# Kernel optimization log

Measured on AMD Instinct MI355X. Metric: run time of the kernel, lower is better.

Reference implementation:

```python
import jax, jax.numpy as jnp
import numpy as np

EPS = 1e-08


def squash(s):
    # s: [B, out_caps, out_d]
    s2 = jnp.sum(s * s, axis=-1, keepdims=True)
    return s2 / (1.0 + s2) * (s / jnp.sqrt(s2 + EPS))


def setup_inputs() -> dict:
    key = jax.random.key(0)
    k1, k2 = jax.random.split(key)
    B, in_caps, out_caps, in_d, out_d = 128, 1152, 32, 8, 16
    u = jax.random.normal(k1, (B, in_caps, in_d), dtype=jnp.float32)
    weight = jax.random.normal(k2, (in_caps, out_caps, in_d, out_d), dtype=jnp.float32)
    return {"u": u, "weight": weight, "iterations": 3}


def reference(u, weight, iterations):
    # u: [B, in_caps, in_d]; weight: [in_caps, out_caps, in_d, out_d]
    u_hat = jnp.einsum('ijnm,bin->bijm', weight, u)  # [B, i, j, m]
    B, in_caps, out_caps, _ = u_hat.shape
    b = jnp.zeros((B, in_caps, out_caps), dtype=u.dtype)
    v = None
    for _ in range(iterations):
        c = jax.nn.softmax(b, axis=1)  # faithful to torch code: softmax over in_caps
        s = jnp.einsum('bij,bijm->bjm', c, u_hat)
        v = squash(s)
        a = jnp.einsum('bjm,bijm->bij', v, u_hat)
        b = b + a
    return v
```

## Files before the change

### kernel.cpp

```cpp
#include <hip/hip_runtime.h>
#include <stdint.h>

constexpr int B_SZ     = 128;
constexpr int IN_CAPS  = 1152;
constexpr int OUT_CAPS = 32;
constexpr int IN_D     = 8;
constexpr int OUT_D    = 16;
constexpr int ITERS    = 3;

constexpr int THREADS  = 1024;
constexpr int NW       = THREADS / 64;
constexpr int G        = 2;
constexpr int TILE_R   = 128;
constexpr int NTILE    = IN_CAPS / TILE_R;
constexpr int ROW_F    = 128;

typedef const uint32_t __attribute__((address_space(1)))* gptr_t;
typedef uint32_t       __attribute__((address_space(3)))* lptr_t;
__device__ __forceinline__ void async_copy16(const float* g, float* l) {
    __builtin_amdgcn_global_load_lds((gptr_t)g, (lptr_t)l, 16, 0, 0);
}

__global__ __launch_bounds__(THREADS) void caps_route(
    const float* __restrict__ u,
    const float* __restrict__ w,
    float* __restrict__ out)
{
    __shared__ __align__(16) float tile[TILE_R * ROW_F];
    __shared__ float red_es[NW * 8];
    __shared__ __align__(16) float red_m[NW * 8 * 4];

    const int nwg = gridDim.x;
    const int bid = blockIdx.x;
    const int wid = (bid & 7) * (nwg >> 3) + (bid >> 3);
    const int j   = wid >> 6;
    const int b0  = (wid & 63) * G;

    const int tid  = threadIdx.x;
    const int lane = tid & 63;
    const int wv   = tid >> 6;
    const int bl   = tid & 1;
    const int mq   = (tid >> 1) & 3;
    const int ir   = tid >> 3;
    const int b    = b0 + bl;

    const int pmir = (ir & 7) ^ ((ir & 1) << 2);
    const int o0   = ((mq ^ pmir) << 2);
    const int o1   = (((4 | mq) ^ pmir) << 2);

    float uh[NTILE][4];
    float4 uA0, uA1;

    #define STAGE_TILE(T)                                                     \
    do {                                                                      \
        _Pragma("unroll")                                                     \
        for (int q = 0; q < 4; ++q) {                                         \
            const int Lb   = (wv * 4 + q) * 64;      \
            const int L    = Lb + lane;                                       \
            const int row  = L >> 5;                                          \
            const int slot = L & 31;                                          \
            const int c    = slot ^ ((row & 7) ^ ((row & 1) << 2));           \
            const float* gsrc = w +                                           \
                ((size_t)(((T) * TILE_R + row) * OUT_CAPS + j) * ROW_F + c * 4); \
            async_copy16(gsrc, &tile[Lb * 4]);                                \
        }                                                                     \
    } while (0)

    #define ULOAD(T)                                                          \
    do {                                                                      \
        const float* up = u + ((size_t)b * IN_CAPS + (T) * TILE_R + ir) * IN_D; \
        uA0 = *reinterpret_cast<const float4*>(up);                           \
        uA1 = *reinterpret_cast<const float4*>(up + 4);                       \
    } while (0)

    #define COMP_TILE(T)                                                      \
    do {                                                                      \
        const float* trow = &tile[ir * ROW_F];                                \
        const float uc[8] = {uA0.x, uA0.y, uA0.z, uA0.w,                      \
                             uA1.x, uA1.y, uA1.z, uA1.w};                     \
        float4 acc = make_float4(0.f, 0.f, 0.f, 0.f);                         \
        _Pragma("unroll")                                                     \
        for (int t = 0; t < 4; ++t) {                                         \
            const float4 wa = *reinterpret_cast<const float4*>(trow + t * 32 + o0); \
            const float4 wb = *reinterpret_cast<const float4*>(trow + t * 32 + o1); \
            acc.x = fmaf(uc[2*t], wa.x, acc.x);                               \
            acc.y = fmaf(uc[2*t], wa.y, acc.y);                               \
            acc.z = fmaf(uc[2*t], wa.z, acc.z);                               \
            acc.w = fmaf(uc[2*t], wa.w, acc.w);                               \
            acc.x = fmaf(uc[2*t+1], wb.x, acc.x);                             \
            acc.y = fmaf(uc[2*t+1], wb.y, acc.y);                             \
            acc.z = fmaf(uc[2*t+1], wb.z, acc.z);                             \
            acc.w = fmaf(uc[2*t+1], wb.w, acc.w);                             \
        }                                                                     \
        uh[(T)][0] = acc.x; uh[(T)][1] = acc.y;                               \
        uh[(T)][2] = acc.z; uh[(T)][3] = acc.w;                               \
    } while (0)

    #define STEP(T)                                                           \
    do {                                                                      \
        __syncthreads();                                                      \
        STAGE_TILE(T);                                                        \
        ULOAD(T);                                                             \
        __syncthreads();                                                      \
        COMP_TILE(T);                                                         \
    } while (0)

    STAGE_TILE(0);
    ULOAD(0);
    __syncthreads();
    COMP_TILE(0);
    STEP(1); STEP(2); STEP(3); STEP(4);
    STEP(5); STEP(6); STEP(7); STEP(8);
    #undef STEP
    #undef COMP_TILE
    #undef ULOAD
    #undef STAGE_TILE

    float e[NTILE];
    #pragma unroll
    for (int r = 0; r < NTILE; ++r) e[r] = 1.0f;
    float vv[4];
    const int grp = lane & 7;

    for (int it = 0; it < ITERS; ++it) {
        float esum = 0.0f;
        #pragma unroll
        for (int r = 0; r < NTILE; ++r) esum += e[r];
        esum += __shfl_xor(esum, 8);
        esum += __shfl_xor(esum, 16);
        esum += __shfl_xor(esum, 32);

        float sp0 = 0.f, sp1 = 0.f, sp2 = 0.f, sp3 = 0.f;
        #pragma unroll
        for (int r = 0; r < NTILE; ++r) {
            sp0 = fmaf(e[r], uh[r][0], sp0);
            sp1 = fmaf(e[r], uh[r][1], sp1);
            sp2 = fmaf(e[r], uh[r][2], sp2);
            sp3 = fmaf(e[r], uh[r][3], sp3);
        }
        sp0 += __shfl_xor(sp0, 8);  sp1 += __shfl_xor(sp1, 8);
        sp2 += __shfl_xor(sp2, 8);  sp3 += __shfl_xor(sp3, 8);
        sp0 += __shfl_xor(sp0, 16); sp1 += __shfl_xor(sp1, 16);
        sp2 += __shfl_xor(sp2, 16); sp3 += __shfl_xor(sp3, 16);
        sp0 += __shfl_xor(sp0, 32); sp1 += __shfl_xor(sp1, 32);
        sp2 += __shfl_xor(sp2, 32); sp3 += __shfl_xor(sp3, 32);

        if (lane < 8) {
            red_es[wv * 8 + lane] = esum;
            *reinterpret_cast<float4*>(&red_m[(wv * 8 + lane) * 4]) =
                make_float4(sp0, sp1, sp2, sp3);
        }
        __syncthreads();
        float gsum = 0.0f;
        float sa0 = 0.f, sa1 = 0.f, sa2 = 0.f, sa3 = 0.f;
        #pragma unroll
        for (int q = 0; q < NW; ++q) {
            gsum += red_es[q * 8 + grp];
            const float4 rm =
                *reinterpret_cast<const float4*>(&red_m[(q * 8 + grp) * 4]);
            sa0 += rm.x; sa1 += rm.y; sa2 += rm.z; sa3 += rm.w;
        }
        __syncthreads();

        const float cinv = 1.0f / gsum;
        vv[0] = sa0 * cinv; vv[1] = sa1 * cinv;
        vv[2] = sa2 * cinv; vv[3] = sa3 * cinv;
        float s2 = fmaf(vv[0], vv[0], fmaf(vv[1], vv[1],
                   fmaf(vv[2], vv[2], vv[3] * vv[3])));
        s2 += __shfl_xor(s2, 2);
        s2 += __shfl_xor(s2, 4);
        const float scale = (s2 / (1.0f + s2)) * rsqrtf(s2 + 1e-8f);
        vv[0] *= scale; vv[1] *= scale; vv[2] *= scale; vv[3] *= scale;

        if (it < ITERS - 1) {
            #pragma unroll
            for (int r = 0; r < NTILE; ++r) {
                float a = fmaf(vv[0], uh[r][0], fmaf(vv[1], uh[r][1],
                          fmaf(vv[2], uh[r][2], vv[3] * uh[r][3])));
                a += __shfl_xor(a, 2);
                a += __shfl_xor(a, 4);
                e[r] *= __expf(a);
            }
        }
    }

    if (tid < 8) {
        float4* op = reinterpret_cast<float4*>(
            out + ((size_t)(b0 + bl) * OUT_CAPS + j) * OUT_D + mq * 4);
        *op = make_float4(vv[0], vv[1], vv[2], vv[3]);
    }
}

extern "C" void kernel_launch(void* const* d_in, const int* in_sizes, int n_in,
                              void* d_out, int out_size, void* d_ws, size_t ws_size,
                              hipStream_t stream) {
    const float* u = (const float*)d_in[0];
    const float* w = (const float*)d_in[1];
    float* out     = (float*)d_out;
    (void)in_sizes; (void)n_in; (void)out_size; (void)d_ws; (void)ws_size;

    dim3 grid(OUT_CAPS * (B_SZ / G));
    dim3 block(THREADS);
    hipLaunchKernelGGL(caps_route, grid, block, 0, stream, u, w, out);
}
```

Measured before the change: 175.0 us.

## Double-buffer weight tiles in LDS as packed bf16 with register staging

```diff
diff --git a/kernel.cpp b/kernel.cpp
--- a/kernel.cpp
+++ b/kernel.cpp
@@ -4,7 +4,6 @@
 constexpr int B_SZ     = 128;
 constexpr int IN_CAPS  = 1152;
 constexpr int OUT_CAPS = 32;
-constexpr int IN_D     = 8;
 constexpr int OUT_D    = 16;
 constexpr int ITERS    = 3;
 
@@ -13,22 +12,15 @@
 constexpr int G        = 2;
 constexpr int TILE_R   = 128;
 constexpr int NTILE    = IN_CAPS / TILE_R;
-constexpr int ROW_F    = 128;
-
-typedef const uint32_t __attribute__((address_space(1)))* gptr_t;
-typedef uint32_t       __attribute__((address_space(3)))* lptr_t;
-__device__ __forceinline__ void async_copy16(const float* g, float* l) {
-    __builtin_amdgcn_global_load_lds((gptr_t)g, (lptr_t)l, 16, 0, 0);
-}
 
 __global__ __launch_bounds__(THREADS) void caps_route(
     const float* __restrict__ u,
     const float* __restrict__ w,
     float* __restrict__ out)
 {
-    __shared__ __align__(16) float tile[TILE_R * ROW_F];
-    __shared__ float red_es[NW * 8];
-    __shared__ __align__(16) float red_m[NW * 8 * 4];
+    __shared__ __align__(16) uint32_t tile[2][TILE_R * 64];
+    __shared__ float red_es[8 * NW];
+    __shared__ __align__(16) float red_m[8 * NW * 4];
 
     const int nwg = gridDim.x;
     const int bid = blockIdx.x;
@@ -42,79 +34,92 @@
     const int bl   = tid & 1;
     const int mq   = (tid >> 1) & 3;
     const int ir   = tid >> 3;
+    const int ir3  = ir & 7;
     const int b    = b0 + bl;
 
-    const int pmir = (ir & 7) ^ ((ir & 1) << 2);
-    const int o0   = ((mq ^ pmir) << 2);
-    const int o1   = (((4 | mq) ^ pmir) << 2);
+    const int srow = tid >> 3;
+    const int sc0  = tid & 7;
 
     float uh[NTILE][4];
-    float4 uA0, uA1;
-
-    #define STAGE_TILE(T)                                                     \
-    do {                                                                      \
-        _Pragma("unroll")                                                     \
-        for (int q = 0; q < 4; ++q) {                                         \
-            const int Lb   = (wv * 4 + q) * 64;      \
-            const int L    = Lb + lane;                                       \
-            const int row  = L >> 5;                                          \
-            const int slot = L & 31;                                          \
-            const int c    = slot ^ ((row & 7) ^ ((row & 1) << 2));           \
-            const float* gsrc = w +                                           \
-                ((size_t)(((T) * TILE_R + row) * OUT_CAPS + j) * ROW_F + c * 4); \
-            async_copy16(gsrc, &tile[Lb * 4]);                                \
-        }                                                                     \
-    } while (0)
-
-    #define ULOAD(T)                                                          \
-    do {                                                                      \
-        const float* up = u + ((size_t)b * IN_CAPS + (T) * TILE_R + ir) * IN_D; \
-        uA0 = *reinterpret_cast<const float4*>(up);                           \
-        uA1 = *reinterpret_cast<const float4*>(up + 4);                       \
-    } while (0)
-
-    #define COMP_TILE(T)                                                      \
-    do {                                                                      \
-        const float* trow = &tile[ir * ROW_F];                                \
-        const float uc[8] = {uA0.x, uA0.y, uA0.z, uA0.w,                      \
-                             uA1.x, uA1.y, uA1.z, uA1.w};                     \
-        float4 acc = make_float4(0.f, 0.f, 0.f, 0.f);                         \
+
+    #define GLOADS(T, C2, RA, RB)                                             \
+    do {                                                                      \
+        const float* gb = w +                                                 \
+            (((size_t)((T) * TILE_R + srow) * OUT_CAPS + j) << 7);            \
+        const int t_ = (C2) >> 2, mqs = (C2) & 3;                             \
+        RA = *reinterpret_cast<const float4*>(gb + t_ * 32 + mqs * 4);        \
+        RB = *reinterpret_cast<const float4*>(gb + t_ * 32 + mqs * 4 + 16);   \
+    } while (0)
+
+    #define PACK_WRITE(NB, C2, RA, RB)                                        \
+    do {                                                                      \
+        uint32_t d0, d1, d2, d3;                                              \
+        asm("v_cvt_pk_bf16_f32 %0, %1, %2" : "=v"(d0) : "v"(RA.x), "v"(RB.x));\
+        asm("v_cvt_pk_bf16_f32 %0, %1, %2" : "=v"(d1) : "v"(RA.y), "v"(RB.y));\
+        asm("v_cvt_pk_bf16_f32 %0, %1, %2" : "=v"(d2) : "v"(RA.z), "v"(RB.z));\
+        asm("v_cvt_pk_bf16_f32 %0, %1, %2" : "=v"(d3) : "v"(RA.w), "v"(RB.w));\
+        const int c_ = (C2) ^ (srow & 7);                                     \
+        *reinterpret_cast<uint4*>(&tile[(NB)][(srow * 16 + c_) * 4]) =        \
+            make_uint4(d0, d1, d2, d3);                                       \
+    } while (0)
+
+    #define COMP(NB, T)                                                       \
+    do {                                                                      \
+        const float* up = u + ((size_t)b * IN_CAPS + (T) * TILE_R + ir) * 8;  \
+        const float4 u0 = *reinterpret_cast<const float4*>(up);               \
+        const float4 u1 = *reinterpret_cast<const float4*>(up + 4);           \
+        const float uc[8] = {u0.x, u0.y, u0.z, u0.w, u1.x, u1.y, u1.z, u1.w}; \
+        float a0 = 0.f, a1 = 0.f, a2 = 0.f, a3 = 0.f;                         \
         _Pragma("unroll")                                                     \
         for (int t = 0; t < 4; ++t) {                                         \
-            const float4 wa = *reinterpret_cast<const float4*>(trow + t * 32 + o0); \
-            const float4 wb = *reinterpret_cast<const float4*>(trow + t * 32 + o1); \
-            acc.x = fmaf(uc[2*t], wa.x, acc.x);                               \
-            acc.y = fmaf(uc[2*t], wa.y, acc.y);                               \
-            acc.z = fmaf(uc[2*t], wa.z, acc.z);                               \
-            acc.w = fmaf(uc[2*t], wa.w, acc.w);                               \
-            acc.x = fmaf(uc[2*t+1], wb.x, acc.x);                             \
-            acc.y = fmaf(uc[2*t+1], wb.y, acc.y);                             \
-            acc.z = fmaf(uc[2*t+1], wb.z, acc.z);                             \
-            acc.w = fmaf(uc[2*t+1], wb.w, acc.w);                             \
+            const int c_ = ((t << 2) | mq) ^ ir3;                             \
+            const uint4 d = *reinterpret_cast<const uint4*>(                  \
+                &tile[(NB)][(ir * 16 + c_) * 4]);                             \
+            const float ue = uc[2 * t], uo = uc[2 * t + 1];                   \
+            a0 = fmaf(ue, __uint_as_float(d.x << 16), a0);                    \
+            a0 = fmaf(uo, __uint_as_float(d.x & 0xffff0000u), a0);            \
+            a1 = fmaf(ue, __uint_as_float(d.y << 16), a1);                    \
+            a1 = fmaf(uo, __uint_as_float(d.y & 0xffff0000u), a1);            \
+            a2 = fmaf(ue, __uint_as_float(d.z << 16), a2);                    \
+            a2 = fmaf(uo, __uint_as_float(d.z & 0xffff0000u), a2);            \
+            a3 = fmaf(ue, __uint_as_float(d.w << 16), a3);                    \
+            a3 = fmaf(uo, __uint_as_float(d.w & 0xffff0000u), a3);            \
         }                                                                     \
-        uh[(T)][0] = acc.x; uh[(T)][1] = acc.y;                               \
-        uh[(T)][2] = acc.z; uh[(T)][3] = acc.w;                               \
+        uh[(T)][0] = a0; uh[(T)][1] = a1;                                     \
+        uh[(T)][2] = a2; uh[(T)][3] = a3;                                     \
     } while (0)
 
     #define STEP(T)                                                           \
     do {                                                                      \
+        if ((T) + 1 < NTILE) {                                                \
+            float4 sA, sB;                                                    \
+            GLOADS((T) + 1, sc0, sA, sB);                                     \
+            COMP((T) & 1, T);                                                 \
+            PACK_WRITE(((T) + 1) & 1, sc0, sA, sB);                           \
+            float4 sC, sD;                                                    \
+            GLOADS((T) + 1, sc0 + 8, sC, sD);                                 \
+            PACK_WRITE(((T) + 1) & 1, sc0 + 8, sC, sD);                       \
+        } else {                                                              \
+            COMP((T) & 1, T);                                                 \
+        }                                                                     \
         __syncthreads();                                                      \
-        STAGE_TILE(T);                                                        \
-        ULOAD(T);                                                             \
-        __syncthreads();                                                      \
-        COMP_TILE(T);                                                         \
-    } while (0)
-
-    STAGE_TILE(0);
-    ULOAD(0);
+    } while (0)
+
+    {
+        float4 sA, sB;
+        GLOADS(0, sc0, sA, sB);
+        PACK_WRITE(0, sc0, sA, sB);
+        GLOADS(0, sc0 + 8, sA, sB);
+        PACK_WRITE(0, sc0 + 8, sA, sB);
+    }
     __syncthreads();
-    COMP_TILE(0);
-    STEP(1); STEP(2); STEP(3); STEP(4);
+
+    STEP(0); STEP(1); STEP(2); STEP(3); STEP(4);
     STEP(5); STEP(6); STEP(7); STEP(8);
     #undef STEP
-    #undef COMP_TILE
-    #undef ULOAD
-    #undef STAGE_TILE
+    #undef COMP
+    #undef PACK_WRITE
+    #undef GLOADS
 
     float e[NTILE];
     #pragma unroll
@@ -146,8 +151,8 @@
         sp2 += __shfl_xor(sp2, 32); sp3 += __shfl_xor(sp3, 32);
 
         if (lane < 8) {
-            red_es[wv * 8 + lane] = esum;
-            *reinterpret_cast<float4*>(&red_m[(wv * 8 + lane) * 4]) =
+            red_es[lane * NW + wv] = esum;
+            *reinterpret_cast<float4*>(&red_m[(lane * NW + wv) * 4]) =
                 make_float4(sp0, sp1, sp2, sp3);
         }
         __syncthreads();
@@ -155,9 +160,9 @@
         float sa0 = 0.f, sa1 = 0.f, sa2 = 0.f, sa3 = 0.f;
         #pragma unroll
         for (int q = 0; q < NW; ++q) {
-            gsum += red_es[q * 8 + grp];
+            gsum += red_es[grp * NW + q];
             const float4 rm =
-                *reinterpret_cast<const float4*>(&red_m[(q * 8 + grp) * 4]);
+                *reinterpret_cast<const float4*>(&red_m[(grp * NW + q) * 4]);
             sa0 += rm.x; sa1 += rm.y; sa2 += rm.z; sa3 += rm.w;
         }
         __syncthreads();
```

Result: slower. 224.7 us (+28.4%).

## Recompute u_hat per routing sweep with accumulated logits and double-buffered weight tiles

Applied to the files above, without the earlier changes.

```diff
diff --git a/kernel.cpp b/kernel.cpp
--- a/kernel.cpp
+++ b/kernel.cpp
@@ -4,16 +4,12 @@
 constexpr int B_SZ     = 128;
 constexpr int IN_CAPS  = 1152;
 constexpr int OUT_CAPS = 32;
-constexpr int IN_D     = 8;
 constexpr int OUT_D    = 16;
-constexpr int ITERS    = 3;
 
-constexpr int THREADS  = 1024;
-constexpr int NW       = THREADS / 64;
-constexpr int G        = 2;
-constexpr int TILE_R   = 128;
+constexpr int THREADS  = 512;
+constexpr int GB       = 8;
+constexpr int TILE_R   = 64;
 constexpr int NTILE    = IN_CAPS / TILE_R;
-constexpr int ROW_F    = 128;
 
 typedef const uint32_t __attribute__((address_space(1)))* gptr_t;
 typedef uint32_t       __attribute__((address_space(3)))* lptr_t;
@@ -21,174 +17,165 @@
     __builtin_amdgcn_global_load_lds((gptr_t)g, (lptr_t)l, 16, 0, 0);
 }
 
-__global__ __launch_bounds__(THREADS) void caps_route(
+__global__ __launch_bounds__(THREADS, 2) void caps_route(
     const float* __restrict__ u,
     const float* __restrict__ w,
     float* __restrict__ out)
 {
-    __shared__ __align__(16) float tile[TILE_R * ROW_F];
-    __shared__ float red_es[NW * 8];
-    __shared__ __align__(16) float red_m[NW * 8 * 4];
+    __shared__ __align__(16) float tile[2][32 * 64 * 4];
+    __shared__ __align__(16) float red[8 * 8 * 20];
+    __shared__ float vlds[GB * OUT_D];
 
     const int nwg = gridDim.x;
     const int bid = blockIdx.x;
     const int wid = (bid & 7) * (nwg >> 3) + (bid >> 3);
-    const int j   = wid >> 6;
-    const int b0  = (wid & 63) * G;
+    const int j   = wid >> 4;
+    const int b0  = (wid & 15) * GB;
 
     const int tid  = threadIdx.x;
     const int lane = tid & 63;
     const int wv   = tid >> 6;
-    const int bl   = tid & 1;
-    const int mq   = (tid >> 1) & 3;
-    const int ir   = tid >> 3;
-    const int b    = b0 + bl;
+    const int b    = tid & 7;
+    const int ipar = tid >> 3;
 
-    const int pmir = (ir & 7) ^ ((ir & 1) << 2);
-    const int o0   = ((mq ^ pmir) << 2);
-    const int o1   = (((4 | mq) ^ pmir) << 2);
+    const float* wj = w + (size_t)j * 128;
+    const float* ub = u + (size_t)(b0 + b) * IN_CAPS * 8;
 
-    float uh[NTILE][4];
-    float4 uA0, uA1;
+    float st[16];
+    float vs[16];
+    float uh[16];
+    float den;
+    float4 ua0, ua1, ub0, ub1;
 
-    #define STAGE_TILE(T)                                                     \
+    #define STAGE(NB, T)                                                      \
     do {                                                                      \
         _Pragma("unroll")                                                     \
         for (int q = 0; q < 4; ++q) {                                         \
-            const int Lb   = (wv * 4 + q) * 64;      \
-            const int L    = Lb + lane;                                       \
-            const int row  = L >> 5;                                          \
-            const int slot = L & 31;                                          \
-            const int c    = slot ^ ((row & 7) ^ ((row & 1) << 2));           \
-            const float* gsrc = w +                                           \
-                ((size_t)(((T) * TILE_R + row) * OUT_CAPS + j) * ROW_F + c * 4); \
-            async_copy16(gsrc, &tile[Lb * 4]);                                \
+            const int c = wv * 4 + q;                                         \
+            const float* gsrc = wj + (size_t)((T) * TILE_R + lane) * 4096 + c * 4; \
+            async_copy16(gsrc, &tile[(NB)][c * 256]);                         \
         }                                                                     \
     } while (0)
 
-    #define ULOAD(T)                                                          \
+    #define ULOAD(T, U0, U1)                                                  \
     do {                                                                      \
-        const float* up = u + ((size_t)b * IN_CAPS + (T) * TILE_R + ir) * IN_D; \
-        uA0 = *reinterpret_cast<const float4*>(up);                           \
-        uA1 = *reinterpret_cast<const float4*>(up + 4);                       \
+        const float* up = ub + (size_t)((T) * TILE_R + ipar) * 8;             \
+        U0 = *reinterpret_cast<const float4*>(up);                            \
+        U1 = *reinterpret_cast<const float4*>(up + 4);                        \
     } while (0)
 
-    #define COMP_TILE(T)                                                      \
+    #define COMP(NB, K, U0, U1)                                               \
     do {                                                                      \
-        const float* trow = &tile[ir * ROW_F];                                \
-        const float uc[8] = {uA0.x, uA0.y, uA0.z, uA0.w,                      \
-                             uA1.x, uA1.y, uA1.z, uA1.w};                     \
-        float4 acc = make_float4(0.f, 0.f, 0.f, 0.f);                         \
+        const float uc[8] = {U0.x, U0.y, U0.z, U0.w, U1.x, U1.y, U1.z, U1.w}; \
         _Pragma("unroll")                                                     \
-        for (int t = 0; t < 4; ++t) {                                         \
-            const float4 wa = *reinterpret_cast<const float4*>(trow + t * 32 + o0); \
-            const float4 wb = *reinterpret_cast<const float4*>(trow + t * 32 + o1); \
-            acc.x = fmaf(uc[2*t], wa.x, acc.x);                               \
-            acc.y = fmaf(uc[2*t], wa.y, acc.y);                               \
-            acc.z = fmaf(uc[2*t], wa.z, acc.z);                               \
-            acc.w = fmaf(uc[2*t], wa.w, acc.w);                               \
-            acc.x = fmaf(uc[2*t+1], wb.x, acc.x);                             \
-            acc.y = fmaf(uc[2*t+1], wb.y, acc.y);                             \
-            acc.z = fmaf(uc[2*t+1], wb.z, acc.z);                             \
-            acc.w = fmaf(uc[2*t+1], wb.w, acc.w);                             \
+        for (int m = 0; m < 16; ++m) uh[m] = 0.0f;                            \
+        _Pragma("unroll")                                                     \
+        for (int c = 0; c < 32; ++c) {                                        \
+            const float4 wc = *reinterpret_cast<const float4*>(               \
+                &tile[(NB)][(c * 64 + ipar) * 4]);                            \
+            const float uv = uc[c >> 2];                                      \
+            const int   mb = (c & 3) * 4;                                     \
+            uh[mb + 0] = fmaf(uv, wc.x, uh[mb + 0]);                          \
+            uh[mb + 1] = fmaf(uv, wc.y, uh[mb + 1]);                          \
+            uh[mb + 2] = fmaf(uv, wc.z, uh[mb + 2]);                          \
+            uh[mb + 3] = fmaf(uv, wc.w, uh[mb + 3]);                          \
         }                                                                     \
-        uh[(T)][0] = acc.x; uh[(T)][1] = acc.y;                               \
-        uh[(T)][2] = acc.z; uh[(T)][3] = acc.w;                               \
+        if ((K) == 0) {                                                       \
+            _Pragma("unroll")                                                 \
+            for (int m = 0; m < 16; ++m) st[m] += uh[m];                      \
+        } else {                                                              \
+            float l0 = vs[0] * uh[0], l1 = vs[1] * uh[1];                     \
+            float l2 = vs[2] * uh[2], l3 = vs[3] * uh[3];                     \
+            _Pragma("unroll")                                                 \
+            for (int m = 4; m < 16; m += 4) {                                 \
+                l0 = fmaf(vs[m + 0], uh[m + 0], l0);                          \
+                l1 = fmaf(vs[m + 1], uh[m + 1], l1);                          \
+                l2 = fmaf(vs[m + 2], uh[m + 2], l2);                          \
+                l3 = fmaf(vs[m + 3], uh[m + 3], l3);                          \
+            }                                                                 \
+            const float e = __expf((l0 + l1) + (l2 + l3));                    \
+            den += e;                                                         \
+            _Pragma("unroll")                                                 \
+            for (int m = 0; m < 16; ++m) st[m] = fmaf(e, uh[m], st[m]);       \
+        }                                                                     \
     } while (0)
 
-    #define STEP(T)                                                           \
+    #define REDUCE(K)                                                         \
     do {                                                                      \
+        _Pragma("unroll")                                                     \
+        for (int m = 0; m < 16; ++m) {                                        \
+            st[m] += __shfl_xor(st[m], 8);                                    \
+            st[m] += __shfl_xor(st[m], 16);                                   \
+            st[m] += __shfl_xor(st[m], 32);                                   \
+        }                                                                     \
+        if ((K) > 0) {                                                        \
+            den += __shfl_xor(den, 8);                                        \
+            den += __shfl_xor(den, 16);                                       \
+            den += __shfl_xor(den, 32);                                       \
+        }                                                                     \
+        if (lane < 8) {                       \
+            float* rb = &red[(wv * 8 + lane) * 20];                           \
+            *reinterpret_cast<float4*>(rb +  0) = make_float4(st[0],  st[1],  st[2],  st[3]);  \
+            *reinterpret_cast<float4*>(rb +  4) = make_float4(st[4],  st[5],  st[6],  st[7]);  \
+            *reinterpret_cast<float4*>(rb +  8) = make_float4(st[8],  st[9],  st[10], st[11]); \
+            *reinterpret_cast<float4*>(rb + 12) = make_float4(st[12], st[13], st[14], st[15]); \
+            rb[16] = den;                                                     \
+        }                                                                     \
         __syncthreads();                                                      \
-        STAGE_TILE(T);                                                        \
-        ULOAD(T);                                                             \
+        if (tid < 128) {                                                      \
+            const int br = tid >> 4, m = tid & 15;                            \
+            float acc = 0.0f, dsum = 0.0f;                                    \
+            _Pragma("unroll")                                                 \
+            for (int q = 0; q < 8; ++q) {                                     \
+                acc  += red[(q * 8 + br) * 20 + m];                           \
+                dsum += red[(q * 8 + br) * 20 + 16];                          \
+            }                                                                 \
+            const float dn = ((K) == 0) ? (float)IN_CAPS : dsum;              \
+            const float sm = acc / dn;                                        \
+            float s2 = sm * sm;                                               \
+            s2 += __shfl_xor(s2, 1); s2 += __shfl_xor(s2, 2);                 \
+            s2 += __shfl_xor(s2, 4); s2 += __shfl_xor(s2, 8);                 \
+            const float v = sm * (s2 / (1.0f + s2)) * rsqrtf(s2 + 1e-8f);     \
+            if ((K) == 0)      vlds[br * 16 + m] = v;                         \
+            else if ((K) == 1) vlds[br * 16 + m] += v;                        \
+            else out[((size_t)(b0 + br) * OUT_CAPS + j) * OUT_D + m] = v;     \
+        }                                                                     \
         __syncthreads();                                                      \
-        COMP_TILE(T);                                                         \
     } while (0)
 
-    STAGE_TILE(0);
-    ULOAD(0);
-    __syncthreads();
-    COMP_TILE(0);
-    STEP(1); STEP(2); STEP(3); STEP(4);
-    STEP(5); STEP(6); STEP(7); STEP(8);
-    #undef STEP
-    #undef COMP_TILE
+    #define SWEEP(K)                                                          \
+    do {                                                                      \
+        if ((K) > 0) {                                                        \
+            _Pragma("unroll")                                                 \
+            for (int m = 0; m < 16; ++m) vs[m] = vlds[b * 16 + m];            \
+        }                                                                     \
+        _Pragma("unroll")                                                     \
+        for (int m = 0; m < 16; ++m) st[m] = 0.0f;                            \
+        den = 0.0f;                                                           \
+        STAGE(0, 0); ULOAD(0, ua0, ua1);                                      \
+        __syncthreads();                                                      \
+        _Pragma("unroll 1")                                                   \
+        for (int t2 = 0; t2 < NTILE / 2; ++t2) {                              \
+            const int Tb = 2 * t2 + 1;                                        \
+            STAGE(1, Tb); ULOAD(Tb, ub0, ub1);                                \
+            COMP(0, K, ua0, ua1);                                             \
+            __syncthreads();                                                  \
+            if (Tb < NTILE - 1) { STAGE(0, Tb + 1); ULOAD(Tb + 1, ua0, ua1); }\
+            COMP(1, K, ub0, ub1);                                             \
+            __syncthreads();                                                  \
+        }                                                                     \
+        REDUCE(K);                                                            \
+    } while (0)
+
+    SWEEP(0);
+    SWEEP(1);
+    SWEEP(2);
+
+    #undef SWEEP
+    #undef REDUCE
+    #undef COMP
     #undef ULOAD
-    #undef STAGE_TILE
-
-    float e[NTILE];
-    #pragma unroll
-    for (int r = 0; r < NTILE; ++r) e[r] = 1.0f;
-    float vv[4];
-    const int grp = lane & 7;
-
-    for (int it = 0; it < ITERS; ++it) {
-        float esum = 0.0f;
-        #pragma unroll
-        for (int r = 0; r < NTILE; ++r) esum += e[r];
-        esum += __shfl_xor(esum, 8);
-        esum += __shfl_xor(esum, 16);
-        esum += __shfl_xor(esum, 32);
-
-        float sp0 = 0.f, sp1 = 0.f, sp2 = 0.f, sp3 = 0.f;
-        #pragma unroll
-        for (int r = 0; r < NTILE; ++r) {
-            sp0 = fmaf(e[r], uh[r][0], sp0);
-            sp1 = fmaf(e[r], uh[r][1], sp1);
-            sp2 = fmaf(e[r], uh[r][2], sp2);
-            sp3 = fmaf(e[r], uh[r][3], sp3);
-        }
-        sp0 += __shfl_xor(sp0, 8);  sp1 += __shfl_xor(sp1, 8);
-        sp2 += __shfl_xor(sp2, 8);  sp3 += __shfl_xor(sp3, 8);
-        sp0 += __shfl_xor(sp0, 16); sp1 += __shfl_xor(sp1, 16);
-        sp2 += __shfl_xor(sp2, 16); sp3 += __shfl_xor(sp3, 16);
-        sp0 += __shfl_xor(sp0, 32); sp1 += __shfl_xor(sp1, 32);
-        sp2 += __shfl_xor(sp2, 32); sp3 += __shfl_xor(sp3, 32);
-
-        if (lane < 8) {
-            red_es[wv * 8 + lane] = esum;
-            *reinterpret_cast<float4*>(&red_m[(wv * 8 + lane) * 4]) =
-                make_float4(sp0, sp1, sp2, sp3);
-        }
-        __syncthreads();
-        float gsum = 0.0f;
-        float sa0 = 0.f, sa1 = 0.f, sa2 = 0.f, sa3 = 0.f;
-        #pragma unroll
-        for (int q = 0; q < NW; ++q) {
-            gsum += red_es[q * 8 + grp];
-            const float4 rm =
-                *reinterpret_cast<const float4*>(&red_m[(q * 8 + grp) * 4]);
-            sa0 += rm.x; sa1 += rm.y; sa2 += rm.z; sa3 += rm.w;
-        }
-        __syncthreads();
-
-        const float cinv = 1.0f / gsum;
-        vv[0] = sa0 * cinv; vv[1] = sa1 * cinv;
-        vv[2] = sa2 * cinv; vv[3] = sa3 * cinv;
-        float s2 = fmaf(vv[0], vv[0], fmaf(vv[1], vv[1],
-                   fmaf(vv[2], vv[2], vv[3] * vv[3])));
-        s2 += __shfl_xor(s2, 2);
-        s2 += __shfl_xor(s2, 4);
-        const float scale = (s2 / (1.0f + s2)) * rsqrtf(s2 + 1e-8f);
-        vv[0] *= scale; vv[1] *= scale; vv[2] *= scale; vv[3] *= scale;
-
-        if (it < ITERS - 1) {
-            #pragma unroll
-            for (int r = 0; r < NTILE; ++r) {
-                float a = fmaf(vv[0], uh[r][0], fmaf(vv[1], uh[r][1],
-                          fmaf(vv[2], uh[r][2], vv[3] * uh[r][3])));
-                a += __shfl_xor(a, 2);
-                a += __shfl_xor(a, 4);
-                e[r] *= __expf(a);
-            }
-        }
-    }
-
-    if (tid < 8) {
-        float4* op = reinterpret_cast<float4*>(
-            out + ((size_t)(b0 + bl) * OUT_CAPS + j) * OUT_D + mq * 4);
-        *op = make_float4(vv[0], vv[1], vv[2], vv[3]);
-    }
+    #undef STAGE
 }
 
 extern "C" void kernel_launch(void* const* d_in, const int* in_sizes, int n_in,
@@ -199,7 +186,7 @@
     float* out     = (float*)d_out;
     (void)in_sizes; (void)n_in; (void)out_size; (void)d_ws; (void)ws_size;
 
-    dim3 grid(OUT_CAPS * (B_SZ / G));
+    dim3 grid(OUT_CAPS * (B_SZ / GB));
     dim3 block(THREADS);
     hipLaunchKernelGGL(caps_route, grid, block, 0, stream, u, w, out);
 }
```

Result: slower. 216.0 us (+23.4%).

## Double-buffer weight and input tiles with async LDS loads and vmcnt waits

Applied to the files above, without the earlier changes.

```diff
diff --git a/kernel.cpp b/kernel.cpp
--- a/kernel.cpp
+++ b/kernel.cpp
@@ -4,7 +4,6 @@
 constexpr int B_SZ     = 128;
 constexpr int IN_CAPS  = 1152;
 constexpr int OUT_CAPS = 32;
-constexpr int IN_D     = 8;
 constexpr int OUT_D    = 16;
 constexpr int ITERS    = 3;
 
@@ -26,7 +25,8 @@
     const float* __restrict__ w,
     float* __restrict__ out)
 {
-    __shared__ __align__(16) float tile[TILE_R * ROW_F];
+    __shared__ __align__(16) float wt[2][TILE_R * ROW_F];
+    __shared__ __align__(16) float ut[2][G * TILE_R * 8];
     __shared__ float red_es[NW * 8];
     __shared__ __align__(16) float red_m[NW * 8 * 4];
 
@@ -42,79 +42,88 @@
     const int bl   = tid & 1;
     const int mq   = (tid >> 1) & 3;
     const int ir   = tid >> 3;
-    const int b    = b0 + bl;
-
-    const int pmir = (ir & 7) ^ ((ir & 1) << 2);
-    const int o0   = ((mq ^ pmir) << 2);
-    const int o1   = (((4 | mq) ^ pmir) << 2);
+
+    const int mir = (ir & 7) | ((ir & 3) << 3);
+    int foff[8];
+    #pragma unroll
+    for (int n = 0; n < 8; ++n) foff[n] = (((4 * n + mq) ^ mir) << 2);
+
+    const float* wj = w + (size_t)j * 128;
 
     float uh[NTILE][4];
-    float4 uA0, uA1;
-
-    #define STAGE_TILE(T)                                                     \
+
+    #define STAGE_W(NB, T)                                                    \
     do {                                                                      \
         _Pragma("unroll")                                                     \
         for (int q = 0; q < 4; ++q) {                                         \
-            const int Lb   = (wv * 4 + q) * 64;      \
+            const int Lb   = (wv * 4 + q) * 64;                               \
             const int L    = Lb + lane;                                       \
             const int row  = L >> 5;                                          \
             const int slot = L & 31;                                          \
-            const int c    = slot ^ ((row & 7) ^ ((row & 1) << 2));           \
-            const float* gsrc = w +                                           \
-                ((size_t)(((T) * TILE_R + row) * OUT_CAPS + j) * ROW_F + c * 4); \
-            async_copy16(gsrc, &tile[Lb * 4]);                                \
-        }                                                                     \
-    } while (0)
-
-    #define ULOAD(T)                                                          \
-    do {                                                                      \
-        const float* up = u + ((size_t)b * IN_CAPS + (T) * TILE_R + ir) * IN_D; \
-        uA0 = *reinterpret_cast<const float4*>(up);                           \
-        uA1 = *reinterpret_cast<const float4*>(up + 4);                       \
-    } while (0)
-
-    #define COMP_TILE(T)                                                      \
-    do {                                                                      \
-        const float* trow = &tile[ir * ROW_F];                                \
-        const float uc[8] = {uA0.x, uA0.y, uA0.z, uA0.w,                      \
-                             uA1.x, uA1.y, uA1.z, uA1.w};                     \
-        float4 acc = make_float4(0.f, 0.f, 0.f, 0.f);                         \
+            const int c    = slot ^ ((row & 7) | ((row & 3) << 3));           \
+            const float* gsrc = wj +                                          \
+                ((size_t)(((T) * TILE_R + row) * OUT_CAPS + j) * 0 +          \
+                 (size_t)((T) * TILE_R + row) * 4096 + c * 4);                \
+            async_copy16(gsrc, &wt[(NB)][Lb * 4]);                            \
+        }                                                                     \
+    } while (0)
+
+    #define STAGE_U(NB, T)                                                    \
+    do {                                                                      \
+        if (wv < 8) {                                                         \
+            const int ubl = wv >> 2;                           \
+            const int q   = wv & 3;                          \
+            const float* gsrc = u +                                           \
+                ((size_t)(b0 + ubl) * IN_CAPS + (T) * TILE_R + q * 32) * 8 +  \
+                lane * 4;                                                     \
+            async_copy16(gsrc, &ut[(NB)][ubl * 1024 + q * 256]);              \
+        }                                                                     \
+    } while (0)
+
+    #define COMP(NB, T)                                                       \
+    do {                                                                      \
+        const float* urow = &ut[(NB)][bl * 1024 + ir * 8];                    \
+        const float4 u0 = *reinterpret_cast<const float4*>(urow);             \
+        const float4 u1 = *reinterpret_cast<const float4*>(urow + 4);         \
+        const float uc[8] = {u0.x, u0.y, u0.z, u0.w, u1.x, u1.y, u1.z, u1.w}; \
+        const float* trow = &wt[(NB)][ir * ROW_F];                            \
+        float a0 = 0.f, a1 = 0.f, a2 = 0.f, a3 = 0.f;                         \
         _Pragma("unroll")                                                     \
-        for (int t = 0; t < 4; ++t) {                                         \
-            const float4 wa = *reinterpret_cast<const float4*>(trow + t * 32 + o0); \
-            const float4 wb = *reinterpret_cast<const float4*>(trow + t * 32 + o1); \
-            acc.x = fmaf(uc[2*t], wa.x, acc.x);                               \
-            acc.y = fmaf(uc[2*t], wa.y, acc.y);                               \
-            acc.z = fmaf(uc[2*t], wa.z, acc.z);                               \
-            acc.w = fmaf(uc[2*t], wa.w, acc.w);                               \
-            acc.x = fmaf(uc[2*t+1], wb.x, acc.x);                             \
-            acc.y = fmaf(uc[2*t+1], wb.y, acc.y);                             \
-            acc.z = fmaf(uc[2*t+1], wb.z, acc.z);                             \
-            acc.w = fmaf(uc[2*t+1], wb.w, acc.w);                             \
-        }                                                                     \
-        uh[(T)][0] = acc.x; uh[(T)][1] = acc.y;                               \
-        uh[(T)][2] = acc.z; uh[(T)][3] = acc.w;                               \
+        for (int n = 0; n < 8; ++n) {                                         \
+            const float4 w4 = *reinterpret_cast<const float4*>(trow + foff[n]); \
+            a0 = fmaf(uc[n], w4.x, a0);                                       \
+            a1 = fmaf(uc[n], w4.y, a1);                                       \
+            a2 = fmaf(uc[n], w4.z, a2);                                       \
+            a3 = fmaf(uc[n], w4.w, a3);                                       \
+        }                                                                     \
+        uh[(T)][0] = a0; uh[(T)][1] = a1;                                     \
+        uh[(T)][2] = a2; uh[(T)][3] = a3;                                     \
     } while (0)
 
     #define STEP(T)                                                           \
     do {                                                                      \
-        __syncthreads();                                                      \
-        STAGE_TILE(T);                                                        \
-        ULOAD(T);                                                             \
-        __syncthreads();                                                      \
-        COMP_TILE(T);                                                         \
-    } while (0)
-
-    STAGE_TILE(0);
-    ULOAD(0);
-    __syncthreads();
-    COMP_TILE(0);
-    STEP(1); STEP(2); STEP(3); STEP(4);
+        if ((T) + 1 < NTILE) {                                                \
+            STAGE_W(((T) + 1) & 1, (T) + 1);                                  \
+            STAGE_U(((T) + 1) & 1, (T) + 1);                                  \
+            if (wv < 8) asm volatile("s_waitcnt vmcnt(5)" ::: "memory");      \
+            else        asm volatile("s_waitcnt vmcnt(4)" ::: "memory");      \
+        } else {                                                              \
+            asm volatile("s_waitcnt vmcnt(0)" ::: "memory");                  \
+        }                                                                     \
+        __builtin_amdgcn_s_barrier();           \
+        __builtin_amdgcn_sched_barrier(0);      \
+        COMP((T) & 1, T);                                                     \
+        __builtin_amdgcn_s_barrier();        \
+    } while (0)
+
+    STAGE_W(0, 0);
+    STAGE_U(0, 0);
+    STEP(0); STEP(1); STEP(2); STEP(3); STEP(4);
     STEP(5); STEP(6); STEP(7); STEP(8);
     #undef STEP
-    #undef COMP_TILE
-    #undef ULOAD
-    #undef STAGE_TILE
+    #undef COMP
+    #undef STAGE_U
+    #undef STAGE_W
 
     float e[NTILE];
     #pragma unroll
```

Measured after the change: 685.9 us. +291.9%, slower.
